# Optimization experiments

Measured on AMD Instinct MI355X. Metric: run time of the kernel, lower is better.

## Reference

```python
import jax, jax.numpy as jnp
import numpy as np

B, S, D = 4, 4096, 64   # batch, seq_len, input_size
H, HD = 4, 16           # num_heads, head_dim


def setup_inputs() -> dict:
    key = jax.random.key(0)
    ks = jax.random.split(key, 9)
    sd = 1.0 / np.sqrt(D)          # torch Linear default uniform(-1/sqrt(fan_in), ...)
    so = 1.0 / np.sqrt(H * HD)
    u = lambda k, shape, s: jax.random.uniform(k, shape, jnp.float32, -s, s)
    return {
        "x": jax.random.normal(ks[0], (B, S, D), jnp.float32),
        "Wq": u(ks[1], (H, D, HD), sd), "bq": u(ks[2], (H, HD), sd),
        "Wk": u(ks[3], (H, D, HD), sd), "bk": u(ks[4], (H, HD), sd),
        "Wv": u(ks[5], (H, D, HD), sd), "bv": u(ks[6], (H, HD), sd),
        "Wo": u(ks[7], (H * HD, D), so), "bo": u(ks[8], (D,), so),
    }


def reference(x, Wq, bq, Wk, bk, Wv, bv, Wo, bo):
    # Batched per-head projections (fuses the original per-head Linear loop)
    q = jnp.einsum('bsd,hde->bhse', x, Wq) + bq[None, :, None, :]
    k = jnp.einsum('bsd,hde->bhse', x, Wk) + bk[None, :, None, :]
    v = jnp.einsum('bsd,hde->bhse', x, Wv) + bv[None, :, None, :]
    # scores: [B, H, S(query), S(key)]
    scores = jnp.einsum('bhse,bhte->bhst', q, k) / np.sqrt(HD).astype(np.float32)
    # FAITHFUL quirk: torch Softmax(dim=1) on [B,S,S] normalizes over the QUERY axis
    w = jax.nn.softmax(scores, axis=2)
    attended = jnp.einsum('bhst,bhte->bhse', w, v)          # [B,H,S,HD]
    concat = attended.transpose(0, 2, 1, 3).reshape(B, S, H * HD)
    out = concat @ Wo + bo                                   # [B,S,D]
    # FAITHFUL quirk: final softmax over the sequence axis (dim=1)
    return jax.nn.softmax(out, axis=1)
```

## Files before the change

kernel.cpp:

```cpp
#include <hip/hip_runtime.h>
#include <hip/hip_bf16.h>


#define BB 4
#define SS 4096
#define DD 64
#define HH 4
#define HDD 16

typedef unsigned int u32;
typedef unsigned short u16;
typedef __attribute__((ext_vector_type(8))) short bfrag;
typedef __attribute__((ext_vector_type(4))) float floatx4;
typedef __attribute__((ext_vector_type(16))) float floatx16;
typedef __attribute__((ext_vector_type(2))) u32 u32x2;
typedef __attribute__((ext_vector_type(4))) u32 u32x4;

#define LOG2E 1.4426950408889634074f
#define QSCALE (LOG2E * 0.25f)

__device__ __forceinline__ float fexp2(float x) {
#if __has_builtin(__builtin_amdgcn_exp2f)
  return __builtin_amdgcn_exp2f(x);
#else
  float r; asm("v_exp_f32 %0, %1" : "=v"(r) : "v"(x)); return r;
#endif
}
__device__ __forceinline__ float frcp(float x) {
#if __has_builtin(__builtin_amdgcn_rcpf)
  return __builtin_amdgcn_rcpf(x);
#else
  float r; asm("v_rcp_f32 %0, %1" : "=v"(r) : "v"(x)); return r;
#endif
}

__device__ __forceinline__ u16 f2bf(float f) {
  u32 u = __builtin_bit_cast(u32, f);
  return (u16)((u + 0x7FFFu + ((u >> 16) & 1u)) >> 16);
}
__device__ __forceinline__ u32 pack_bf(float lo, float hi) {
#if __has_builtin(__builtin_amdgcn_perm)
  return __builtin_amdgcn_perm(__builtin_bit_cast(u32, hi),
                               __builtin_bit_cast(u32, lo), 0x07060302u);
#else
  u32 a = __builtin_bit_cast(u32, lo);
  u32 b = __builtin_bit_cast(u32, hi);
  return (a >> 16) | (b & 0xFFFF0000u);
#endif
}

__global__ __launch_bounds__(256) void k_proj(
    const float* __restrict__ x,
    const float* __restrict__ Wq, const float* __restrict__ bq,
    const float* __restrict__ Wk, const float* __restrict__ bk,
    const float* __restrict__ Wv, const float* __restrict__ bv,
    u16* __restrict__ qb, u16* __restrict__ kb, float* __restrict__ vf)
{
  __shared__ float xs[16 * 64];
  const int tid = threadIdx.x;
  const int blk = blockIdx.x;
  const int b   = blk >> 8;
  const int s0  = (blk & 255) << 4;
  ((float4*)xs)[tid] = ((const float4*)(x + ((size_t)b * SS + s0) * DD))[tid];
  __syncthreads();

  const int col = tid & 63, h = col >> 4, e = col & 15;
  const int rg  = tid >> 6;
  float aq[4] = {0,0,0,0}, ak[4] = {0,0,0,0}, av[4] = {0,0,0,0};
  const int wofs = h * (DD * HDD) + e;
#pragma unroll 4
  for (int d = 0; d < DD; ++d) {
    float wq = Wq[wofs + d * HDD];
    float wk = Wk[wofs + d * HDD];
    float wv = Wv[wofs + d * HDD];
    const float* xr = xs + (rg * 4) * 64 + d;
#pragma unroll
    for (int r = 0; r < 4; ++r) {
      float xv = xr[r * 64];
      aq[r] += xv * wq; ak[r] += xv * wk; av[r] += xv * wv;
    }
  }
  const float bqv = bq[col], bkv = bk[col], bvv = bv[col];
  size_t base = ((size_t)(b * HH + h) * SS + (s0 + rg * 4)) * HDD + e;
#pragma unroll
  for (int r = 0; r < 4; ++r) {
    qb[base + r * HDD] = f2bf((aq[r] + bqv) * QSCALE);
    kb[base + r * HDD] = f2bf(ak[r] + bkv);
    vf[base + r * HDD] = av[r] + bvv;
  }
}

__global__ __launch_bounds__(256, 8) void k_colsum(
    const u16* __restrict__ qb, const u16* __restrict__ kb,
    float* __restrict__ csp)
{
  const int tid = threadIdx.x;
  const int lane = tid & 63, w = tid >> 6;
  const int l31 = lane & 31, hl = lane >> 5;
  const int bh = blockIdx.z, chunk = blockIdx.y;
  const int t0 = blockIdx.x * 128 + w * 32;
  const size_t base = (size_t)bh * (SS * HDD);

  const bfrag kf = *(const bfrag*)(kb + base + (size_t)(t0 + l31) * HDD + hl * 8);
  const u16* qp = qb + base + (size_t)l31 * HDD + hl * 8;
  const floatx16 z16 = {0.f};
  float c = 0.f;
  const int s0 = chunk * 1024;
#pragma unroll 2
  for (int s = s0; s < s0 + 1024; s += 32) {
    bfrag qfr = *(const bfrag*)(qp + (size_t)s * HDD);
    floatx16 d = __builtin_amdgcn_mfma_f32_32x32x16_bf16(qfr, kf, z16, 0, 0, 0);
#pragma unroll
    for (int i = 0; i < 16; ++i) c += fexp2(d[i]);
  }
  c += __shfl_xor(c, 32, 64);
  if (hl == 0)
    csp[((size_t)bh * 4 + chunk) * SS + t0 + l31] = c;
}

__global__ __launch_bounds__(256) void k_vprep(
    const float* __restrict__ vf, const float* __restrict__ csp,
    u16* __restrict__ vt)
{
  __shared__ u16 tr[16][264];
  __shared__ float rcs[256];
  const int tid = threadIdx.x;
  const int bh  = blockIdx.y;
  const int t0  = blockIdx.x << 8;
  {
    size_t o = (size_t)bh * 4 * SS + t0 + tid;
    rcs[tid] = frcp(csp[o] + csp[o + SS] + csp[o + 2 * SS] + csp[o + 3 * SS]);
  }
  __syncthreads();
  const float* vsrc = vf + ((size_t)bh * SS + t0) * HDD;
#pragma unroll 4
  for (int i = 0; i < 16; ++i) {
    int idx = (i << 8) + tid;
    int tl = idx >> 4, e2 = idx & 15;
    tr[e2][tl] = f2bf(vsrc[idx] * rcs[tl]);
  }
  __syncthreads();
  u16* dst = vt + (size_t)bh * HDD * SS + t0;
#pragma unroll 4
  for (int j = 0; j < 16; ++j)
    dst[(size_t)j * SS + tid] = tr[j][tid];
}

__global__ __launch_bounds__(256, 4) void k_attn(
    const u16* __restrict__ qb, const u16* __restrict__ kb,
    const u16* __restrict__ vt, float* __restrict__ attp)
{
  __shared__ __align__(16) u16 vls[16 * 1032];
  const int tid  = threadIdx.x;
  const int lane = tid & 63, w = tid >> 6;
  const int l31 = lane & 31, hl = lane >> 5;
  const int bh = blockIdx.z, b = bh >> 2, h = bh & 3;
  const int tp = blockIdx.y;
  const int s0 = blockIdx.x * 128 + w * 32;
  const size_t base = (size_t)bh * (SS * HDD);
  const int tb = tp * 1024;

  {
    const u16* vsrc = vt + (size_t)bh * HDD * SS + tb;
#pragma unroll
    for (int kk = 0; kk < 8; ++kk) {
      int c = tid + 256 * kk;
      int row = c >> 7, rem = c & 127, ii = rem >> 2, g = rem & 3;
      u32x4 vv = *(const u32x4*)(vsrc + (size_t)row * SS + ii * 32 + g * 8);
      u16* wp = vls + row * 1032 + ii * 32 + g * 4;
      *(u32x2*)wp        = (u32x2){vv.x, vv.y};
      *(u32x2*)(wp + 16) = (u32x2){vv.z, vv.w};
    }
  }
  __syncthreads();

  const bfrag qf = *(const bfrag*)(qb + base + (size_t)(s0 + l31) * HDD + hl * 8);
  const u16* kp = kb + base + (size_t)l31 * HDD + hl * 8;
  const u16* vrow = vls + (l31 & 15) * 1032 + hl * 16;

  floatx16 acc = {0.f};
  const floatx16 z16 = {0.f};

#pragma unroll 2
  for (int it = 0; it < 32; ++it) {
    bfrag kf = *(const bfrag*)(kp + (size_t)(tb + it * 32) * HDD);
    floatx16 d = __builtin_amdgcn_mfma_f32_32x32x16_bf16(kf, qf, z16, 0, 0, 0);
    u32 wr[8];
#pragma unroll
    for (int p = 0; p < 8; ++p)
      wr[p] = pack_bf(fexp2(d[2 * p]), fexp2(d[2 * p + 1]));
    const u16* va = vrow + it * 32;
    u32x4 af0 = *(const u32x4*)(va);
    u32x4 af1 = *(const u32x4*)(va + 8);
    u32x4 ef0 = {wr[0], wr[1], wr[2], wr[3]};
    u32x4 ef1 = {wr[4], wr[5], wr[6], wr[7]};
    acc = __builtin_amdgcn_mfma_f32_32x32x16_bf16(
        __builtin_bit_cast(bfrag, af0), __builtin_bit_cast(bfrag, ef0), acc, 0, 0, 0);
    acc = __builtin_amdgcn_mfma_f32_32x32x16_bf16(
        __builtin_bit_cast(bfrag, af1), __builtin_bit_cast(bfrag, ef1), acc, 0, 0, 0);
  }

  float* ao = attp + (((size_t)tp * BB + b) * SS + s0 + l31) * (HH * HDD)
            + h * HDD + 4 * hl;
  float4 lo4 = {acc[0], acc[1], acc[2], acc[3]};
  float4 hi4 = {acc[4], acc[5], acc[6], acc[7]};
  *(float4*)ao       = lo4;
  *(float4*)(ao + 8) = hi4;
}

__global__ __launch_bounds__(256) void k_oproj(
    const float* __restrict__ att, const float* __restrict__ Wo,
    const float* __restrict__ bo, float* __restrict__ outp,
    float* __restrict__ part)
{
  __shared__ float wols[64 * 64];
  __shared__ float red[4][64];
  const int tid = threadIdx.x;
  const int blk = blockIdx.x;
  const int b = blk >> 9, s0 = (blk & 511) << 3;
#pragma unroll
  for (int i = 0; i < 4; ++i)
    ((float4*)wols)[tid + 256 * i] = ((const float4*)Wo)[tid + 256 * i];
  __syncthreads();

  const int d = tid & 63, sg = tid >> 6;
  const float bov = bo[d];
  const size_t so = (size_t)BB * SS * 16;
  float es = 0.f;
#pragma unroll
  for (int r = 0; r < 2; ++r) {
    int s = s0 + sg * 2 + r;
    const floatx4* row = (const floatx4*)(att + ((size_t)b * SS + s) * 64);
    float acc = bov;
#pragma unroll
    for (int j = 0; j < 16; ++j) {
      floatx4 c = row[j] + row[j + so] + row[j + 2 * so] + row[j + 3 * so];
      acc += c[0] * wols[(4*j+0)*64 + d] + c[1] * wols[(4*j+1)*64 + d]
           + c[2] * wols[(4*j+2)*64 + d] + c[3] * wols[(4*j+3)*64 + d];
    }
    outp[((size_t)b * SS + s) * 64 + d] = acc;
    es += fexp2(acc * LOG2E);
  }
  red[sg][d] = es;
  __syncthreads();
  if (tid < 64)
    part[((size_t)b * 512 + (blk & 511)) * 64 + tid] =
        red[0][tid] + red[1][tid] + red[2][tid] + red[3][tid];
}

__global__ __launch_bounds__(256) void k_softmax(
    const float* __restrict__ outp, const float* __restrict__ part,
    float* __restrict__ out)
{
  __shared__ float red[4][64];
  __shared__ float rs[64];
  const int tid = threadIdx.x, d = tid & 63, sg = tid >> 6;
  const int st = blockIdx.x;
  const int b = blockIdx.y;
  {
    float e = 0.f;
    const float* pp = part + ((size_t)b * 512 + sg * 128) * 64 + d;
#pragma unroll 8
    for (int c = 0; c < 128; ++c) e += pp[c * 64];
    red[sg][d] = e;
  }
  __syncthreads();
  if (tid < 64)
    rs[tid] = frcp(red[0][tid] + red[1][tid] + red[2][tid] + red[3][tid]);
  __syncthreads();
  const float r = rs[d];
  const size_t rowbase = ((size_t)b * SS + st * 64 + sg * 16) * 64 + d;
#pragma unroll 4
  for (int i = 0; i < 16; ++i)
    out[rowbase + i * 64] = fexp2(outp[rowbase + i * 64] * LOG2E) * r;
}

extern "C" void kernel_launch(void* const* d_in, const int* in_sizes, int n_in,
                              void* d_out, int out_size, void* d_ws, size_t ws_size,
                              hipStream_t stream) {
  const float* x  = (const float*)d_in[0];
  const float* Wq = (const float*)d_in[1];
  const float* bq = (const float*)d_in[2];
  const float* Wk = (const float*)d_in[3];
  const float* bk = (const float*)d_in[4];
  const float* Wv = (const float*)d_in[5];
  const float* bv = (const float*)d_in[6];
  const float* Wo = (const float*)d_in[7];
  const float* bo = (const float*)d_in[8];

  char* ws = (char*)d_ws;
  constexpr size_t QB_OFF  = 0;
  constexpr size_t KB_OFF  = (size_t)2  << 20;
  constexpr size_t VF_OFF  = (size_t)4  << 20;
  constexpr size_t VT_OFF  = (size_t)8  << 20;
  constexpr size_t CSP_OFF = (size_t)10 << 20;
  constexpr size_t ATT_OFF = (size_t)11 << 20;
  constexpr size_t OUT_OFF = (size_t)27 << 20;
  constexpr size_t PT_OFF  = (size_t)31 << 20;

  u16*   qb   = (u16*)  (ws + QB_OFF);
  u16*   kb   = (u16*)  (ws + KB_OFF);
  float* vf   = (float*)(ws + VF_OFF);
  u16*   vt   = (u16*)  (ws + VT_OFF);
  float* csp  = (float*)(ws + CSP_OFF);
  float* attp = (float*)(ws + ATT_OFF);
  float* outp = (float*)(ws + OUT_OFF);
  float* part = (float*)(ws + PT_OFF);
  float* out  = (float*)d_out;

  hipLaunchKernelGGL(k_proj,    dim3(1024),       dim3(256), 0, stream,
                     x, Wq, bq, Wk, bk, Wv, bv, qb, kb, vf);
  hipLaunchKernelGGL(k_colsum,  dim3(32, 4, 16),  dim3(256), 0, stream, qb, kb, csp);
  hipLaunchKernelGGL(k_vprep,   dim3(16, 16),     dim3(256), 0, stream, vf, csp, vt);
  hipLaunchKernelGGL(k_attn,    dim3(32, 4, 16),  dim3(256), 0, stream, qb, kb, vt, attp);
  hipLaunchKernelGGL(k_oproj,   dim3(2048),       dim3(256), 0, stream,
                     attp, Wo, bo, outp, part);
  hipLaunchKernelGGL(k_softmax, dim3(64, 4),      dim3(256), 0, stream, outp, part, out);
}
```

Measured before the change: 197.8 us.

## Fuse all stages into one cooperative persistent kernel with grid syncs

Replaces the six separate kernel launches with a single cooperative kernel of 1024 blocks that runs projection, column-sum, V normalisation, attention, output projection and final softmax, separated by grid-wide barriers. The V normalisation and transpose is folded into the attention stage's shared-memory load, so the vt buffer is no longer used on this path. Each block now handles two work units in the colsum, attention and oproj stages. This removes launch gaps and the separate vprep pass, at the cost of grid.sync overhead, 4 blocks per CU required for co-residency, and fewer blocks in flight for the heavy attention stage. If the cooperative launch fails, the old multi-kernel path is used.

```diff
diff --git a/kernel.cpp b/kernel.cpp
--- a/kernel.cpp
+++ b/kernel.cpp
@@ -1,6 +1,9 @@
 #include <hip/hip_runtime.h>
 #include <hip/hip_bf16.h>
-
+#include <hip/hip_cooperative_groups.h>
+
+
+namespace cg = cooperative_groups;
 
 #define BB 4
 #define SS 4096
@@ -49,6 +52,214 @@
 #endif
 }
 
+__global__ __launch_bounds__(256, 4) void k_mha(
+    const float* __restrict__ x,
+    const float* __restrict__ Wq, const float* __restrict__ bq,
+    const float* __restrict__ Wk, const float* __restrict__ bk,
+    const float* __restrict__ Wv, const float* __restrict__ bv,
+    const float* __restrict__ Wo, const float* __restrict__ bo,
+    u16* __restrict__ qb, u16* __restrict__ kb, float* __restrict__ vf,
+    float* __restrict__ csp, float* __restrict__ attp,
+    float* __restrict__ outp, float* __restrict__ part,
+    float* __restrict__ out)
+{
+  __shared__ __align__(16) char smem[33152];
+  cg::grid_group grid = cg::this_grid();
+  const int tid  = threadIdx.x;
+  const int blk  = blockIdx.x;
+  const int lane = tid & 63, w = tid >> 6;
+
+  {
+    float* xs = (float*)smem;
+    const int b  = blk >> 8;
+    const int s0 = (blk & 255) << 4;
+    ((float4*)xs)[tid] = ((const float4*)(x + ((size_t)b * SS + s0) * DD))[tid];
+    __syncthreads();
+
+    const int col = tid & 63, h = col >> 4, e = col & 15;
+    const int rg  = tid >> 6;
+    float aq[4] = {0,0,0,0}, ak[4] = {0,0,0,0}, av[4] = {0,0,0,0};
+    const int wofs = h * (DD * HDD) + e;
+#pragma unroll 4
+    for (int d = 0; d < DD; ++d) {
+      float wq = Wq[wofs + d * HDD];
+      float wk = Wk[wofs + d * HDD];
+      float wv = Wv[wofs + d * HDD];
+      const float* xr = xs + (rg * 4) * 64 + d;
+#pragma unroll
+      for (int r = 0; r < 4; ++r) {
+        float xv = xr[r * 64];
+        aq[r] += xv * wq; ak[r] += xv * wk; av[r] += xv * wv;
+      }
+    }
+    const float bqv = bq[col], bkv = bk[col], bvv = bv[col];
+    size_t base = ((size_t)(b * HH + h) * SS + (s0 + rg * 4)) * HDD + e;
+#pragma unroll
+    for (int r = 0; r < 4; ++r) {
+      qb[base + r * HDD] = f2bf((aq[r] + bqv) * QSCALE);
+      kb[base + r * HDD] = f2bf(ak[r] + bkv);
+      vf[base + r * HDD] = av[r] + bvv;
+    }
+  }
+  grid.sync();
+
+  {
+    const int l31 = lane & 31, hl = lane >> 5;
+    const floatx16 z16 = {0.f};
+#pragma unroll
+    for (int j = 0; j < 2; ++j) {
+      const int unit = 2 * blk + j;
+      const int tgrp = unit & 31, chunk = (unit >> 5) & 3, bh = unit >> 7;
+      const int t0 = tgrp * 128 + w * 32;
+      const size_t base = (size_t)bh * (SS * HDD);
+      const bfrag kf = *(const bfrag*)(kb + base + (size_t)(t0 + l31) * HDD + hl * 8);
+      const u16* qp = qb + base + (size_t)l31 * HDD + hl * 8;
+      float c = 0.f;
+      const int s0 = chunk * 1024;
+#pragma unroll 2
+      for (int s = s0; s < s0 + 1024; s += 32) {
+        bfrag qfr = *(const bfrag*)(qp + (size_t)s * HDD);
+        floatx16 d = __builtin_amdgcn_mfma_f32_32x32x16_bf16(qfr, kf, z16, 0, 0, 0);
+#pragma unroll
+        for (int i = 0; i < 16; ++i) c += fexp2(d[i]);
+      }
+      c += __shfl_xor(c, 32, 64);
+      if (hl == 0)
+        csp[((size_t)bh * 4 + chunk) * SS + t0 + l31] = c;
+    }
+  }
+  grid.sync();
+
+  {
+    u16* vls = (u16*)smem;
+    const int p = blk & 15, tp = (blk >> 4) & 3, bh = blk >> 6;
+    const int b = bh >> 2, h = bh & 3;
+    const int tb = tp * 1024;
+    const size_t base = (size_t)bh * (SS * HDD);
+
+    __syncthreads();
+    {
+      const float4* vsrc = (const float4*)(vf + base + (size_t)tb * HDD);
+      const float* cp0 = csp + (size_t)bh * 4 * SS + tb;
+#pragma unroll
+      for (int kk = 0; kk < 16; ++kk) {
+        int c = kk * 256 + tid;
+        int tl = c >> 2, g = c & 3;
+        float4 vv = vsrc[c];
+        float rc = frcp(cp0[tl] + cp0[tl + SS] + cp0[tl + 2 * SS] + cp0[tl + 3 * SS]);
+        int i5 = tl >> 5, t5 = tl & 31;
+        int sub = ((t5 >> 2) & 1) * 16 + ((t5 >> 3) << 2) + (t5 & 3);
+        u16* wp = vls + i5 * 32 + sub;
+        wp[(4 * g + 0) * 1032] = f2bf(vv.x * rc);
+        wp[(4 * g + 1) * 1032] = f2bf(vv.y * rc);
+        wp[(4 * g + 2) * 1032] = f2bf(vv.z * rc);
+        wp[(4 * g + 3) * 1032] = f2bf(vv.w * rc);
+      }
+    }
+    __syncthreads();
+
+    const int l31 = lane & 31, hl = lane >> 5;
+    const u16* kp = kb + base + (size_t)l31 * HDD + hl * 8;
+    const u16* vrow = vls + (l31 & 15) * 1032 + hl * 16;
+    const floatx16 z16 = {0.f};
+
+#pragma unroll
+    for (int j = 0; j < 2; ++j) {
+      const int s0 = p * 256 + j * 128 + w * 32;
+      const bfrag qf = *(const bfrag*)(qb + base + (size_t)(s0 + l31) * HDD + hl * 8);
+      floatx16 acc = {0.f};
+#pragma unroll 2
+      for (int it = 0; it < 32; ++it) {
+        bfrag kf = *(const bfrag*)(kp + (size_t)(tb + it * 32) * HDD);
+        floatx16 d = __builtin_amdgcn_mfma_f32_32x32x16_bf16(kf, qf, z16, 0, 0, 0);
+        u32 wr[8];
+#pragma unroll
+        for (int pp = 0; pp < 8; ++pp)
+          wr[pp] = pack_bf(fexp2(d[2 * pp]), fexp2(d[2 * pp + 1]));
+        const u16* va = vrow + it * 32;
+        u32x4 af0 = *(const u32x4*)(va);
+        u32x4 af1 = *(const u32x4*)(va + 8);
+        u32x4 ef0 = {wr[0], wr[1], wr[2], wr[3]};
+        u32x4 ef1 = {wr[4], wr[5], wr[6], wr[7]};
+        acc = __builtin_amdgcn_mfma_f32_32x32x16_bf16(
+            __builtin_bit_cast(bfrag, af0), __builtin_bit_cast(bfrag, ef0), acc, 0, 0, 0);
+        acc = __builtin_amdgcn_mfma_f32_32x32x16_bf16(
+            __builtin_bit_cast(bfrag, af1), __builtin_bit_cast(bfrag, ef1), acc, 0, 0, 0);
+      }
+      float* ao = attp + (((size_t)tp * BB + b) * SS + s0 + l31) * (HH * HDD)
+                + h * HDD + 4 * hl;
+      float4 lo4 = {acc[0], acc[1], acc[2], acc[3]};
+      float4 hi4 = {acc[4], acc[5], acc[6], acc[7]};
+      *(float4*)ao       = lo4;
+      *(float4*)(ao + 8) = hi4;
+    }
+  }
+  grid.sync();
+
+  {
+    float* wols = (float*)smem;
+    float* red  = (float*)(smem + 16384);
+#pragma unroll
+    for (int i = 0; i < 4; ++i)
+      ((float4*)wols)[tid + 256 * i] = ((const float4*)Wo)[tid + 256 * i];
+
+    const int d = tid & 63, sg = tid >> 6;
+    const float bov = bo[d];
+    const size_t so = (size_t)BB * SS * 16;
+#pragma unroll
+    for (int j = 0; j < 2; ++j) {
+      const int unit = 2 * blk + j;
+      const int b = unit >> 9, s0 = (unit & 511) << 3;
+      __syncthreads();
+      float es = 0.f;
+#pragma unroll
+      for (int r = 0; r < 2; ++r) {
+        int s = s0 + sg * 2 + r;
+        const floatx4* row = (const floatx4*)(attp + ((size_t)b * SS + s) * 64);
+        float acc = bov;
+#pragma unroll
+        for (int jj = 0; jj < 16; ++jj) {
+          floatx4 c = row[jj] + row[jj + so] + row[jj + 2 * so] + row[jj + 3 * so];
+          acc += c[0] * wols[(4*jj+0)*64 + d] + c[1] * wols[(4*jj+1)*64 + d]
+               + c[2] * wols[(4*jj+2)*64 + d] + c[3] * wols[(4*jj+3)*64 + d];
+        }
+        outp[((size_t)b * SS + s) * 64 + d] = acc;
+        es += fexp2(acc * LOG2E);
+      }
+      red[sg * 64 + d] = es;
+      __syncthreads();
+      if (tid < 64)
+        part[((size_t)b * 512 + (unit & 511)) * 64 + tid] =
+            red[tid] + red[64 + tid] + red[128 + tid] + red[192 + tid];
+    }
+  }
+  grid.sync();
+
+  if (blk < 256) {
+    float* red = (float*)smem;
+    float* rs  = (float*)(smem + 1024);
+    const int d = tid & 63, sg = tid >> 6;
+    const int st = blk & 63, b = blk >> 6;
+    __syncthreads();
+    {
+      float e = 0.f;
+      const float* pp = part + ((size_t)b * 512 + sg * 128) * 64 + d;
+#pragma unroll 8
+      for (int c = 0; c < 128; ++c) e += pp[c * 64];
+      red[sg * 64 + d] = e;
+    }
+    __syncthreads();
+    if (tid < 64)
+      rs[tid] = frcp(red[tid] + red[64 + tid] + red[128 + tid] + red[192 + tid]);
+    __syncthreads();
+    const float r = rs[d];
+    const size_t rowbase = ((size_t)b * SS + st * 64 + sg * 16) * 64 + d;
+#pragma unroll 4
+    for (int i = 0; i < 16; ++i)
+      out[rowbase + i * 64] = fexp2(outp[rowbase + i * 64] * LOG2E) * r;
+  }
+}
+
 __global__ __launch_bounds__(256) void k_proj(
     const float* __restrict__ x,
     const float* __restrict__ Wq, const float* __restrict__ bq,
@@ -63,7 +274,6 @@
   const int s0  = (blk & 255) << 4;
   ((float4*)xs)[tid] = ((const float4*)(x + ((size_t)b * SS + s0) * DD))[tid];
   __syncthreads();
-
   const int col = tid & 63, h = col >> 4, e = col & 15;
   const int rg  = tid >> 6;
   float aq[4] = {0,0,0,0}, ak[4] = {0,0,0,0}, av[4] = {0,0,0,0};
@@ -100,7 +310,6 @@
   const int bh = blockIdx.z, chunk = blockIdx.y;
   const int t0 = blockIdx.x * 128 + w * 32;
   const size_t base = (size_t)bh * (SS * HDD);
-
   const bfrag kf = *(const bfrag*)(kb + base + (size_t)(t0 + l31) * HDD + hl * 8);
   const u16* qp = qb + base + (size_t)l31 * HDD + hl * 8;
   const floatx16 z16 = {0.f};
@@ -159,7 +368,6 @@
   const int s0 = blockIdx.x * 128 + w * 32;
   const size_t base = (size_t)bh * (SS * HDD);
   const int tb = tp * 1024;
-
   {
     const u16* vsrc = vt + (size_t)bh * HDD * SS + tb;
 #pragma unroll
@@ -173,14 +381,11 @@
     }
   }
   __syncthreads();
-
   const bfrag qf = *(const bfrag*)(qb + base + (size_t)(s0 + l31) * HDD + hl * 8);
   const u16* kp = kb + base + (size_t)l31 * HDD + hl * 8;
   const u16* vrow = vls + (l31 & 15) * 1032 + hl * 16;
-
   floatx16 acc = {0.f};
   const floatx16 z16 = {0.f};
-
 #pragma unroll 2
   for (int it = 0; it < 32; ++it) {
     bfrag kf = *(const bfrag*)(kp + (size_t)(tb + it * 32) * HDD);
@@ -199,7 +404,6 @@
     acc = __builtin_amdgcn_mfma_f32_32x32x16_bf16(
         __builtin_bit_cast(bfrag, af1), __builtin_bit_cast(bfrag, ef1), acc, 0, 0, 0);
   }
-
   float* ao = attp + (((size_t)tp * BB + b) * SS + s0 + l31) * (HH * HDD)
             + h * HDD + 4 * hl;
   float4 lo4 = {acc[0], acc[1], acc[2], acc[3]};
@@ -222,7 +426,6 @@
   for (int i = 0; i < 4; ++i)
     ((float4*)wols)[tid + 256 * i] = ((const float4*)Wo)[tid + 256 * i];
   __syncthreads();
-
   const int d = tid & 63, sg = tid >> 6;
   const float bov = bo[d];
   const size_t so = (size_t)BB * SS * 16;
@@ -308,12 +511,20 @@
   float* part = (float*)(ws + PT_OFF);
   float* out  = (float*)d_out;
 
-  hipLaunchKernelGGL(k_proj,    dim3(1024),       dim3(256), 0, stream,
-                     x, Wq, bq, Wk, bk, Wv, bv, qb, kb, vf);
-  hipLaunchKernelGGL(k_colsum,  dim3(32, 4, 16),  dim3(256), 0, stream, qb, kb, csp);
-  hipLaunchKernelGGL(k_vprep,   dim3(16, 16),     dim3(256), 0, stream, vf, csp, vt);
-  hipLaunchKernelGGL(k_attn,    dim3(32, 4, 16),  dim3(256), 0, stream, qb, kb, vt, attp);
-  hipLaunchKernelGGL(k_oproj,   dim3(2048),       dim3(256), 0, stream,
-                     attp, Wo, bo, outp, part);
-  hipLaunchKernelGGL(k_softmax, dim3(64, 4),      dim3(256), 0, stream, outp, part, out);
-}
+  void* args[] = { (void*)&x, (void*)&Wq, (void*)&bq, (void*)&Wk, (void*)&bk,
+                   (void*)&Wv, (void*)&bv, (void*)&Wo, (void*)&bo,
+                   (void*)&qb, (void*)&kb, (void*)&vf, (void*)&csp,
+                   (void*)&attp, (void*)&outp, (void*)&part, (void*)&out };
+  hipError_t err = hipLaunchCooperativeKernel((const void*)k_mha, dim3(1024),
+                                              dim3(256), args, 0, stream);
+  if (err != hipSuccess) {
+    hipLaunchKernelGGL(k_proj,    dim3(1024),      dim3(256), 0, stream,
+                       x, Wq, bq, Wk, bk, Wv, bv, qb, kb, vf);
+    hipLaunchKernelGGL(k_colsum,  dim3(32, 4, 16), dim3(256), 0, stream, qb, kb, csp);
+    hipLaunchKernelGGL(k_vprep,   dim3(16, 16),    dim3(256), 0, stream, vf, csp, vt);
+    hipLaunchKernelGGL(k_attn,    dim3(32, 4, 16), dim3(256), 0, stream, qb, kb, vt, attp);
+    hipLaunchKernelGGL(k_oproj,   dim3(2048),      dim3(256), 0, stream,
+                       attp, Wo, bo, outp, part);
+    hipLaunchKernelGGL(k_softmax, dim3(64, 4),     dim3(256), 0, stream, outp, part, out);
+  }
+}
```

Measured after the change: 700.6 us. 3.54x slower.

## Fuse V normalization/transpose into attention kernel and halve key-split partials

Applied to the files above, without the earlier changes.

Removes the separate k_vprep kernel; each attention block now reads fp32 V and column-sum partials directly, computes reciprocal column sums and writes scaled bf16 V transposed into LDS itself. The key dimension is split into 2 partitions of 2048 (each block loops over two 1024-key chunks) instead of 4, so the attention partial output and the oproj reduction read half as many partials. This drops one launch and one global round trip, but each block redoes V scaling per chunk, adds extra barriers, and the grid is halved, which may reduce parallelism; scattered 2-byte LDS stores may bank-conflict.

```diff
diff --git a/kernel.cpp b/kernel.cpp
--- a/kernel.cpp
+++ b/kernel.cpp
@@ -118,89 +118,79 @@
     csp[((size_t)bh * 4 + chunk) * SS + t0 + l31] = c;
 }
 
-__global__ __launch_bounds__(256) void k_vprep(
-    const float* __restrict__ vf, const float* __restrict__ csp,
-    u16* __restrict__ vt)
-{
-  __shared__ u16 tr[16][264];
-  __shared__ float rcs[256];
-  const int tid = threadIdx.x;
-  const int bh  = blockIdx.y;
-  const int t0  = blockIdx.x << 8;
-  {
-    size_t o = (size_t)bh * 4 * SS + t0 + tid;
-    rcs[tid] = frcp(csp[o] + csp[o + SS] + csp[o + 2 * SS] + csp[o + 3 * SS]);
-  }
-  __syncthreads();
-  const float* vsrc = vf + ((size_t)bh * SS + t0) * HDD;
-#pragma unroll 4
-  for (int i = 0; i < 16; ++i) {
-    int idx = (i << 8) + tid;
-    int tl = idx >> 4, e2 = idx & 15;
-    tr[e2][tl] = f2bf(vsrc[idx] * rcs[tl]);
-  }
-  __syncthreads();
-  u16* dst = vt + (size_t)bh * HDD * SS + t0;
-#pragma unroll 4
-  for (int j = 0; j < 16; ++j)
-    dst[(size_t)j * SS + tid] = tr[j][tid];
-}
-
 __global__ __launch_bounds__(256, 4) void k_attn(
     const u16* __restrict__ qb, const u16* __restrict__ kb,
-    const u16* __restrict__ vt, float* __restrict__ attp)
+    const float* __restrict__ vf, const float* __restrict__ csp,
+    float* __restrict__ attp)
 {
   __shared__ __align__(16) u16 vls[16 * 1032];
+  __shared__ float rcs[1024];
   const int tid  = threadIdx.x;
   const int lane = tid & 63, w = tid >> 6;
   const int l31 = lane & 31, hl = lane >> 5;
   const int bh = blockIdx.z, b = bh >> 2, h = bh & 3;
-  const int tp = blockIdx.y;
+  const int tph = blockIdx.y;
   const int s0 = blockIdx.x * 128 + w * 32;
   const size_t base = (size_t)bh * (SS * HDD);
-  const int tb = tp * 1024;
-
-  {
-    const u16* vsrc = vt + (size_t)bh * HDD * SS + tb;
-#pragma unroll
-    for (int kk = 0; kk < 8; ++kk) {
-      int c = tid + 256 * kk;
-      int row = c >> 7, rem = c & 127, ii = rem >> 2, g = rem & 3;
-      u32x4 vv = *(const u32x4*)(vsrc + (size_t)row * SS + ii * 32 + g * 8);
-      u16* wp = vls + row * 1032 + ii * 32 + g * 4;
-      *(u32x2*)wp        = (u32x2){vv.x, vv.y};
-      *(u32x2*)(wp + 16) = (u32x2){vv.z, vv.w};
-    }
-  }
-  __syncthreads();
 
   const bfrag qf = *(const bfrag*)(qb + base + (size_t)(s0 + l31) * HDD + hl * 8);
   const u16* kp = kb + base + (size_t)l31 * HDD + hl * 8;
   const u16* vrow = vls + (l31 & 15) * 1032 + hl * 16;
-
+  const floatx16 z16 = {0.f};
   floatx16 acc = {0.f};
-  const floatx16 z16 = {0.f};
+
+  for (int th = 0; th < 2; ++th) {
+    const int tb = (tph * 2 + th) * 1024;
+    __syncthreads();
+    {
+      const float* cp0 = csp + (size_t)bh * 4 * SS + tb;
+#pragma unroll
+      for (int i = 0; i < 4; ++i) {
+        int j = i * 256 + tid;
+        rcs[j] = frcp(cp0[j] + cp0[j + SS] + cp0[j + 2 * SS] + cp0[j + 3 * SS]);
+      }
+    }
+    __syncthreads();
+    {
+      const float4* vsrc = (const float4*)(vf + base + (size_t)tb * HDD);
+#pragma unroll
+      for (int kk = 0; kk < 16; ++kk) {
+        int c = kk * 256 + tid;
+        int tl = c >> 2, g = c & 3;
+        float4 vv = vsrc[c];
+        float rc = rcs[tl];
+        int i5 = tl >> 5, t5 = tl & 31;
+        int sub = ((t5 >> 2) & 1) * 16 + ((t5 >> 3) << 2) + (t5 & 3);
+        u16* wp = vls + i5 * 32 + sub;
+        wp[(4 * g + 0) * 1032] = f2bf(vv.x * rc);
+        wp[(4 * g + 1) * 1032] = f2bf(vv.y * rc);
+        wp[(4 * g + 2) * 1032] = f2bf(vv.z * rc);
+        wp[(4 * g + 3) * 1032] = f2bf(vv.w * rc);
+      }
+    }
+    __syncthreads();
 
 #pragma unroll 2
-  for (int it = 0; it < 32; ++it) {
-    bfrag kf = *(const bfrag*)(kp + (size_t)(tb + it * 32) * HDD);
-    floatx16 d = __builtin_amdgcn_mfma_f32_32x32x16_bf16(kf, qf, z16, 0, 0, 0);
-    u32 wr[8];
-#pragma unroll
-    for (int p = 0; p < 8; ++p)
-      wr[p] = pack_bf(fexp2(d[2 * p]), fexp2(d[2 * p + 1]));
-    const u16* va = vrow + it * 32;
-    u32x4 af0 = *(const u32x4*)(va);
-    u32x4 af1 = *(const u32x4*)(va + 8);
-    u32x4 ef0 = {wr[0], wr[1], wr[2], wr[3]};
-    u32x4 ef1 = {wr[4], wr[5], wr[6], wr[7]};
-    acc = __builtin_amdgcn_mfma_f32_32x32x16_bf16(
-        __builtin_bit_cast(bfrag, af0), __builtin_bit_cast(bfrag, ef0), acc, 0, 0, 0);
-    acc = __builtin_amdgcn_mfma_f32_32x32x16_bf16(
-        __builtin_bit_cast(bfrag, af1), __builtin_bit_cast(bfrag, ef1), acc, 0, 0, 0);
-  }
-
-  float* ao = attp + (((size_t)tp * BB + b) * SS + s0 + l31) * (HH * HDD)
+    for (int it = 0; it < 32; ++it) {
+      bfrag kf = *(const bfrag*)(kp + (size_t)(tb + it * 32) * HDD);
+      floatx16 d = __builtin_amdgcn_mfma_f32_32x32x16_bf16(kf, qf, z16, 0, 0, 0);
+      u32 wr[8];
+#pragma unroll
+      for (int p = 0; p < 8; ++p)
+        wr[p] = pack_bf(fexp2(d[2 * p]), fexp2(d[2 * p + 1]));
+      const u16* va = vrow + it * 32;
+      u32x4 af0 = *(const u32x4*)(va);
+      u32x4 af1 = *(const u32x4*)(va + 8);
+      u32x4 ef0 = {wr[0], wr[1], wr[2], wr[3]};
+      u32x4 ef1 = {wr[4], wr[5], wr[6], wr[7]};
+      acc = __builtin_amdgcn_mfma_f32_32x32x16_bf16(
+          __builtin_bit_cast(bfrag, af0), __builtin_bit_cast(bfrag, ef0), acc, 0, 0, 0);
+      acc = __builtin_amdgcn_mfma_f32_32x32x16_bf16(
+          __builtin_bit_cast(bfrag, af1), __builtin_bit_cast(bfrag, ef1), acc, 0, 0, 0);
+    }
+  }
+
+  float* ao = attp + (((size_t)tph * BB + b) * SS + s0 + l31) * (HH * HDD)
             + h * HDD + 4 * hl;
   float4 lo4 = {acc[0], acc[1], acc[2], acc[3]};
   float4 hi4 = {acc[4], acc[5], acc[6], acc[7]};
@@ -234,7 +224,7 @@
     float acc = bov;
 #pragma unroll
     for (int j = 0; j < 16; ++j) {
-      floatx4 c = row[j] + row[j + so] + row[j + 2 * so] + row[j + 3 * so];
+      floatx4 c = row[j] + row[j + so];
       acc += c[0] * wols[(4*j+0)*64 + d] + c[1] * wols[(4*j+1)*64 + d]
            + c[2] * wols[(4*j+2)*64 + d] + c[3] * wols[(4*j+3)*64 + d];
     }
@@ -292,7 +282,6 @@
   constexpr size_t QB_OFF  = 0;
   constexpr size_t KB_OFF  = (size_t)2  << 20;
   constexpr size_t VF_OFF  = (size_t)4  << 20;
-  constexpr size_t VT_OFF  = (size_t)8  << 20;
   constexpr size_t CSP_OFF = (size_t)10 << 20;
   constexpr size_t ATT_OFF = (size_t)11 << 20;
   constexpr size_t OUT_OFF = (size_t)27 << 20;
@@ -301,7 +290,6 @@
   u16*   qb   = (u16*)  (ws + QB_OFF);
   u16*   kb   = (u16*)  (ws + KB_OFF);
   float* vf   = (float*)(ws + VF_OFF);
-  u16*   vt   = (u16*)  (ws + VT_OFF);
   float* csp  = (float*)(ws + CSP_OFF);
   float* attp = (float*)(ws + ATT_OFF);
   float* outp = (float*)(ws + OUT_OFF);
@@ -311,8 +299,8 @@
   hipLaunchKernelGGL(k_proj,    dim3(1024),       dim3(256), 0, stream,
                      x, Wq, bq, Wk, bk, Wv, bv, qb, kb, vf);
   hipLaunchKernelGGL(k_colsum,  dim3(32, 4, 16),  dim3(256), 0, stream, qb, kb, csp);
-  hipLaunchKernelGGL(k_vprep,   dim3(16, 16),     dim3(256), 0, stream, vf, csp, vt);
-  hipLaunchKernelGGL(k_attn,    dim3(32, 4, 16),  dim3(256), 0, stream, qb, kb, vt, attp);
+  hipLaunchKernelGGL(k_attn,    dim3(32, 2, 16),  dim3(256), 0, stream,
+                     qb, kb, vf, csp, attp);
   hipLaunchKernelGGL(k_oproj,   dim3(2048),       dim3(256), 0, stream,
                      attp, Wo, bo, outp, part);
   hipLaunchKernelGGL(k_softmax, dim3(64, 4),      dim3(256), 0, stream, outp, part, out);
```

New measurement: 195.1 us. Within noise of the previous version (-1.4%).
